# Optimization experiments

Hardware: AMD Instinct MI355X
Metric: run time of the kernel (lower is better)

The kernel has to match this reference:

```python
import jax, jax.numpy as jnp
import numpy as np

D_MODEL = 512
H = 8
DK = D_MODEL // H  # 64


def setup_inputs() -> dict:
    key = jax.random.key(0)
    ks = jax.random.split(key, 8)
    B, S = 2, 4096
    q = jax.random.normal(ks[0], (B, S, D_MODEL), dtype=jnp.float32)
    k = jax.random.normal(ks[1], (B, S, D_MODEL), dtype=jnp.float32)
    v = jax.random.normal(ks[2], (B, S, D_MODEL), dtype=jnp.float32)
    # per-head projection weights, torch nn.Linear layout [out, in], stacked over heads
    scale = 1.0 / np.sqrt(D_MODEL)
    Wq = jax.random.uniform(ks[3], (H, DK, D_MODEL), jnp.float32, -scale, scale)
    Wk = jax.random.uniform(ks[4], (H, DK, D_MODEL), jnp.float32, -scale, scale)
    Wv = jax.random.uniform(ks[5], (H, DK, D_MODEL), jnp.float32, -scale, scale)
    Wo = jax.random.uniform(ks[6], (D_MODEL, D_MODEL), jnp.float32, -scale, scale)
    # causal mask (True = keep), matches masked_fill(mask.logical_not(), -inf)
    mask = jnp.tril(jnp.ones((S, S), dtype=jnp.bool_))
    return {"q": q, "k": k, "v": v, "Wq": Wq, "Wk": Wk, "Wv": Wv, "Wo": Wo, "mask": mask}


def reference(q, k, v, Wq, Wk, Wv, Wo, mask):
    # per-head projections (stacked): x @ W^T for each head -> [B, H, S, DK]
    qh = jnp.einsum('bsd,hed->bhse', q, Wq)
    kh = jnp.einsum('bsd,hed->bhse', k, Wk)
    vh = jnp.einsum('bsd,hed->bhse', v, Wv)
    scaling = 1.0 / np.sqrt(DK)
    scores = jnp.einsum('bhse,bhte->bhst', qh, kh) * scaling  # [B,H,S,S]
    scores = jnp.where(mask, scores, -jnp.inf)
    attn = jax.nn.softmax(scores, axis=-1)
    heads = jnp.einsum('bhst,bhte->bhse', attn, vh)  # [B,H,S,DK]
    B, _, S, _ = heads.shape
    concat = jnp.transpose(heads, (0, 2, 1, 3)).reshape(B, S, D_MODEL)
    return concat @ Wo.T
```

## Files before the change

kernel.cpp:

```cpp
#include <hip/hip_runtime.h>
#include <hip/hip_bf16.h>
#include <math.h>

typedef __bf16 bf16_t;
typedef __bf16 bf16x8 __attribute__((ext_vector_type(8)));
typedef __bf16 bf16x4 __attribute__((ext_vector_type(4)));
typedef short short4v __attribute__((ext_vector_type(4)));
typedef float f32x4 __attribute__((ext_vector_type(4)));

__device__ __forceinline__ f32x4 mfma_k32(bf16x8 a, bf16x8 b, f32x4 c) {
    return __builtin_amdgcn_mfma_f32_16x16x32_bf16(a, b, c, 0, 0, 0);
}

__device__ __forceinline__ f32x4 mfma_k16(bf16x4 a, bf16x4 b, f32x4 c) {
#if __has_builtin(__builtin_amdgcn_mfma_f32_16x16x16_bf16)
    return __builtin_amdgcn_mfma_f32_16x16x16_bf16(a, b, c, 0, 0, 0);
#elif __has_builtin(__builtin_amdgcn_mfma_f32_16x16x16bf16_1k)
    short4v as, bs;
    __builtin_memcpy(&as, &a, 8);
    __builtin_memcpy(&bs, &b, 8);
    return __builtin_amdgcn_mfma_f32_16x16x16bf16_1k(as, bs, c, 0, 0, 0);
#else
    f32x4 d = c;
    asm volatile("v_mfma_f32_16x16x16_bf16 %0, %1, %2, %0" : "+v"(d) : "v"(a), "v"(b));
    return d;
#endif
}

__device__ __forceinline__ float fast_exp2(float x) {
#if __has_builtin(__builtin_amdgcn_exp2f)
    return __builtin_amdgcn_exp2f(x);
#else
    float r;
    asm("v_exp_f32 %0, %1" : "=v"(r) : "v"(x));
    return r;
#endif
}

__device__ __forceinline__ void async16(const bf16_t* g, __bf16* l) {
    __builtin_amdgcn_global_load_lds(
        (const __attribute__((address_space(1))) void*)g,
        (__attribute__((address_space(3))) void*)l, 16, 0, 0);
}

__device__ __forceinline__ int swz_col(int col, int row) {
    return (col & ~63) | ((((col >> 3) & 7) ^ (row & 7)) << 3) | (col & 7);
}

__global__ __launch_bounds__(256) void cvt_all(const float* __restrict__ q,
                                               const float* __restrict__ k,
                                               const float* __restrict__ v,
                                               const float* __restrict__ Wq,
                                               const float* __restrict__ Wk,
                                               const float* __restrict__ Wv,
                                               const float* __restrict__ Wo,
                                               bf16_t* __restrict__ qc,
                                               bf16_t* __restrict__ kc,
                                               bf16_t* __restrict__ vc,
                                               bf16_t* __restrict__ Wc) {
    const int bx = blockIdx.x;
    if (bx < 2048) {
        size_t i = ((size_t)bx * 256 + threadIdx.x) * 8;
        int row = (int)(i >> 9), col = (int)(i & 511);
        size_t di = (size_t)row * 512 + swz_col(col, row);
        float4 a0 = *(const float4*)(q + i), a1 = *(const float4*)(q + i + 4);
        float4 b0 = *(const float4*)(k + i), b1 = *(const float4*)(k + i + 4);
        float4 c0 = *(const float4*)(v + i), c1 = *(const float4*)(v + i + 4);
        bf16x8 qo, ko, vo;
        qo[0]=(__bf16)a0.x; qo[1]=(__bf16)a0.y; qo[2]=(__bf16)a0.z; qo[3]=(__bf16)a0.w;
        qo[4]=(__bf16)a1.x; qo[5]=(__bf16)a1.y; qo[6]=(__bf16)a1.z; qo[7]=(__bf16)a1.w;
        ko[0]=(__bf16)b0.x; ko[1]=(__bf16)b0.y; ko[2]=(__bf16)b0.z; ko[3]=(__bf16)b0.w;
        ko[4]=(__bf16)b1.x; ko[5]=(__bf16)b1.y; ko[6]=(__bf16)b1.z; ko[7]=(__bf16)b1.w;
        vo[0]=(__bf16)c0.x; vo[1]=(__bf16)c0.y; vo[2]=(__bf16)c0.z; vo[3]=(__bf16)c0.w;
        vo[4]=(__bf16)c1.x; vo[5]=(__bf16)c1.y; vo[6]=(__bf16)c1.z; vo[7]=(__bf16)c1.w;
        *(bf16x8*)(qc + di) = qo;
        *(bf16x8*)(kc + di) = ko;
        *(bf16x8*)(vc + di) = vo;
    } else {
        const int b2 = bx - 2048;
        const int m = b2 >> 7;
        const float* src = m == 0 ? Wq : m == 1 ? Wk : m == 2 ? Wv : Wo;
        const float sc = (m == 0) ? 0.125f * 1.44269504088896f : 1.0f;
        size_t i = ((size_t)(b2 & 127) * 256 + threadIdx.x) * 8;
        int row = (int)(i >> 9), col = (int)(i & 511);
        float4 a0 = *(const float4*)(src + i), a1 = *(const float4*)(src + i + 4);
        bf16x8 o;
        o[0]=(__bf16)(a0.x*sc); o[1]=(__bf16)(a0.y*sc); o[2]=(__bf16)(a0.z*sc); o[3]=(__bf16)(a0.w*sc);
        o[4]=(__bf16)(a1.x*sc); o[5]=(__bf16)(a1.y*sc); o[6]=(__bf16)(a1.z*sc); o[7]=(__bf16)(a1.w*sc);
        *(bf16x8*)(Wc + (size_t)m * 262144 + (size_t)row * 512 + swz_col(col, row)) = o;
    }
}

template<int MODE>
__device__ __forceinline__ void gemm128_body(const bf16_t* __restrict__ A,
                                             const bf16_t* __restrict__ B,
                                             void* __restrict__ outp,
                                             int m0, int n0) {
    __shared__ __bf16 Asm[128 * 64];
    __shared__ __bf16 Bsm[128 * 64];
    const int tid  = threadIdx.x;
    const int wave = tid >> 6;
    const int lane = tid & 63;
    const int quad = lane >> 4;
    const int l16  = lane & 15;
    const int swz  = l16 & 7;
    const int r8 = lane >> 3;
    const int c8 = (lane & 7) * 8;
    const int mrow0 = (wave & 1) * 64;
    const int ncol0 = (wave >> 1) * 64;

    f32x4 acc[4][4];
    for (int i = 0; i < 4; ++i)
        for (int j = 0; j < 4; ++j) acc[i][j] = (f32x4){0.f, 0.f, 0.f, 0.f};

    for (int kt = 0; kt < 512; kt += 64) {
        __syncthreads();
        for (int j = 0; j < 4; ++j) {
            async16(A + (size_t)(m0 + wave * 32 + j * 8 + r8) * 512 + kt + c8,
                    &Asm[(wave * 32 + j * 8) * 64]);
            async16(B + (size_t)(n0 + wave * 32 + j * 8 + r8) * 512 + kt + c8,
                    &Bsm[(wave * 32 + j * 8) * 64]);
        }
        __syncthreads();

        for (int ks = 0; ks < 2; ++ks) {
            bf16x8 af[4];
            for (int mt = 0; mt < 4; ++mt)
                af[mt] = *(const bf16x8*)&Asm[(mrow0 + mt * 16 + l16) * 64 + ((ks * 4 + quad) ^ swz) * 8];
            for (int nt = 0; nt < 4; ++nt) {
                bf16x8 bf = *(const bf16x8*)&Bsm[(ncol0 + nt * 16 + l16) * 64 + ((ks * 4 + quad) ^ swz) * 8];
                for (int mt = 0; mt < 4; ++mt)
                    acc[mt][nt] = mfma_k32(af[mt], bf, acc[mt][nt]);
            }
        }
    }

    if (MODE == 0) {
        bf16_t* out = (bf16_t*)outp;
        for (int nt = 0; nt < 4; ++nt) {
            int e = n0 + ncol0 + nt * 16 + l16;
            int h = e >> 6, el = e & 63;
            for (int mt = 0; mt < 4; ++mt)
                for (int r = 0; r < 4; ++r) {
                    int row = m0 + mrow0 + mt * 16 + quad * 4 + r;
                    int b = row >> 12, s = row & 4095;
                    int elp = (((el >> 3) ^ (row & 7)) << 3) | (el & 7);
                    out[(((size_t)(b * 8 + h)) * 4096 + s) * 64 + elp] = (bf16_t)acc[mt][nt][r];
                }
        }
    } else if (MODE == 1) {
        bf16_t* out = (bf16_t*)outp;
        for (int nt = 0; nt < 4; ++nt) {
            int s_g = n0 + ncol0 + nt * 16 + l16;
            int b = s_g >> 12;
            int sbase = (s_g & 4095) & ~63;
            int f = 16 * ((l16 >> 2) & 3) + 4 * nt + (l16 & 3);
            for (int mt = 0; mt < 4; ++mt)
                for (int r = 0; r < 4; ++r) {
                    int e_g = m0 + mrow0 + mt * 16 + quad * 4 + r;
                    int h = e_g >> 6, el = e_g & 63;
                    int col = sbase | ((((f >> 3) ^ (e_g & 7)) & 7) << 3) | (f & 7);
                    out[(((size_t)(b * 8 + h)) * 64 + el) * 4096 + col] = (bf16_t)acc[mt][nt][r];
                }
        }
    } else {
        float* out = (float*)outp;
        for (int nt = 0; nt < 4; ++nt) {
            int n = n0 + ncol0 + nt * 16 + l16;
            for (int mt = 0; mt < 4; ++mt)
                for (int r = 0; r < 4; ++r) {
                    int row = m0 + mrow0 + mt * 16 + quad * 4 + r;
                    out[(size_t)row * 512 + n] = acc[mt][nt][r];
                }
        }
    }
}

__global__ __launch_bounds__(256) void proj_fused(const bf16_t* __restrict__ xs,
                                                  const bf16_t* __restrict__ Wc,
                                                  bf16_t* __restrict__ qh,
                                                  bf16_t* __restrict__ kh,
                                                  bf16_t* __restrict__ vh) {
    const int z = blockIdx.z;
    const bf16_t* X = xs + (size_t)z * 4194304;
    const bf16_t* W = Wc + (size_t)z * 262144;
    if (z == 0)
        gemm128_body<0>(X, W, qh, blockIdx.x * 128, blockIdx.y * 128);
    else if (z == 1)
        gemm128_body<0>(X, W, kh, blockIdx.x * 128, blockIdx.y * 128);
    else
        gemm128_body<1>(W, X, vh, blockIdx.y * 128, blockIdx.x * 128);
}

__global__ __launch_bounds__(256) void gemm_final(const bf16_t* __restrict__ A,
                                                  const bf16_t* __restrict__ B,
                                                  float* __restrict__ out) {
    gemm128_body<2>(A, B, out, blockIdx.x * 128, blockIdx.y * 128);
}

__global__ __launch_bounds__(256, 4) void attn_kernel(const bf16_t* __restrict__ qh,
                                                      const bf16_t* __restrict__ kh,
                                                      const bf16_t* __restrict__ vh,
                                                      bf16_t* __restrict__ Opart,
                                                      float* __restrict__ Lpart) {
    __shared__ __bf16 SM[16384];
    __bf16* KSM = &SM[0];
    __bf16* VSM = &SM[8192];
    float* Osc = (float*)SM;
    float* Lsc = (float*)&SM[8192];

    const int id   = blockIdx.x;
    const int bh   = ((id & 7) << 1) | ((id >> 3) & 1);
    const int pair = (id >> 4) & 31;
    const int z    = (id >> 9) & 1;

    const int tid  = threadIdx.x;
    const int wave = tid >> 6;
    const int g2   = wave >> 1;
    const int wl   = wave & 1;
    const int lane = tid & 63;
    const int quad = lane >> 4;
    const int l16  = lane & 15;
    const int swz  = l16 & 7;
    const size_t base = (size_t)bh * 4096 * 64;
    const int r8 = lane >> 3;
    const int c8 = (lane & 7) * 8;

    bf16_t* Op = Opart + (size_t)z * 4194304;
    float*  Lp = Lpart + z * 65536;

    for (int leg = 0; leg < 2; ++leg) {
        const int qt = leg ? (63 - pair) : pair;
        const int q0 = qt * 64;

        bf16x8 qf[2][2];
        for (int g = 0; g < 2; ++g) {
            const bf16_t* qp = qh + base + (size_t)(q0 + wl * 32 + g * 16 + l16) * 64;
            qf[g][0] = *(const bf16x8*)(qp + ((quad ^ swz) * 8));
            qf[g][1] = *(const bf16x8*)(qp + (((4 + quad) ^ swz) * 8));
        }

        f32x4 o[2][4];
        for (int g = 0; g < 2; ++g)
            for (int i = 0; i < 4; ++i) o[g][i] = (f32x4){0.f, 0.f, 0.f, 0.f};
        float lsum[2] = {0.f, 0.f};

        const int S  = (qt + 2) >> 1;
        const int Sh = (S + 1) >> 1;
        const int it0 = z ? Sh : 0;
        const int it1 = z ? S : Sh;

        for (int it = it0; it < it1; ++it) {
            const int j0 = it * 128;
            __syncthreads();
            for (int p = 0; p < 2; ++p)
                for (int j = 0; j < 2; ++j) {
                    int row = wave * 16 + j * 8 + r8;
                    async16(kh + base + (size_t)(j0 + p * 64 + row) * 64 + c8,
                            KSM + (p * 64 + wave * 16 + j * 8) * 64);
                    async16(vh + (size_t)(bh * 64 + row) * 4096 + j0 + p * 64 + c8,
                            VSM + (p * 64 + wave * 16 + j * 8) * 64);
                }
            __syncthreads();

            const int pp = g2;
            const int koff = j0 + pp * 64 - q0;
            if (koff > wl * 32 + 31) continue;

            f32x4 st[2][4];
            for (int nt = 0; nt < 4; ++nt) {
                const __bf16* kr = KSM + (pp * 64 + nt * 16 + l16) * 64;
                bf16x8 kf0 = *(const bf16x8*)(kr + ((quad ^ swz) * 8));
                bf16x8 kf1 = *(const bf16x8*)(kr + (((4 + quad) ^ swz) * 8));
                for (int g = 0; g < 2; ++g) {
                    f32x4 zz = (f32x4){0.f, 0.f, 0.f, 0.f};
                    zz = mfma_k32(kf0, qf[g][0], zz);
                    zz = mfma_k32(kf1, qf[g][1], zz);
                    st[g][nt] = zz;
                }
            }

            bf16x4 pf[2][4];
            for (int g = 0; g < 2; ++g) {
                const int qb = wl * 32 + g * 16;
                if (koff + 63 <= qb) {
                    for (int nt = 0; nt < 4; ++nt)
                        for (int r = 0; r < 4; ++r) {
                            float p = fast_exp2(st[g][nt][r]);
                            lsum[g] += p;
                            pf[g][nt][r] = (bf16_t)p;
                        }
                } else {
                    const int qrow = qb + l16;
                    for (int nt = 0; nt < 4; ++nt)
                        for (int r = 0; r < 4; ++r) {
                            int key = nt * 16 + quad * 4 + r;
                            float p = (key + koff <= qrow) ? fast_exp2(st[g][nt][r]) : 0.f;
                            lsum[g] += p;
                            pf[g][nt][r] = (bf16_t)p;
                        }
                }
            }

            for (int dt = 0; dt < 4; ++dt)
                for (int kt2 = 0; kt2 < 2; ++kt2) {
                    bf16x8 vf = *(const bf16x8*)&VSM[(pp * 64 + dt * 16 + l16) * 64 + (((2 * quad + kt2) ^ swz) * 8)];
                    bf16x4 vlo = {vf[0], vf[1], vf[2], vf[3]};
                    bf16x4 vhi = {vf[4], vf[5], vf[6], vf[7]};
                    for (int g = 0; g < 2; ++g) {
                        o[g][dt] = mfma_k16(pf[g][2 * kt2], vlo, o[g][dt]);
                        o[g][dt] = mfma_k16(pf[g][2 * kt2 + 1], vhi, o[g][dt]);
                    }
                }
        }

        __syncthreads();
        if (g2 == 1) {
            for (int g = 0; g < 2; ++g) {
                float ls = lsum[g];
                ls += __shfl_xor(ls, 16);
                ls += __shfl_xor(ls, 32);
                const int qb = wl * 32 + g * 16;
                Lsc[qb + l16] = ls;
                for (int dt = 0; dt < 4; ++dt)
                    for (int r = 0; r < 4; ++r)
                        Osc[(qb + quad * 4 + r) * 64 + dt * 16 + l16] = o[g][dt][r];
            }
        }
        __syncthreads();
        if (g2 == 0) {
            for (int g = 0; g < 2; ++g) {
                float ls = lsum[g];
                ls += __shfl_xor(ls, 16);
                ls += __shfl_xor(ls, 32);
                const int qb = wl * 32 + g * 16;
                ls += Lsc[qb + l16];
                Lsc[qb + l16] = ls;
                for (int dt = 0; dt < 4; ++dt)
                    for (int r = 0; r < 4; ++r) {
                        int idx = (qb + quad * 4 + r) * 64 + dt * 16 + l16;
                        Osc[idx] = o[g][dt][r] + Osc[idx];
                    }
            }
        }
        __syncthreads();
        {
            const int q  = tid >> 2;
            const int e0 = (tid & 3) * 16;
            bf16x8 w0, w1;
            for (int i = 0; i < 8; ++i) {
                w0[i] = (bf16_t)Osc[q * 64 + e0 + i];
                w1[i] = (bf16_t)Osc[q * 64 + e0 + 8 + i];
            }
            size_t slot = ((size_t)(bh * 64 + qt)) * 4096 + q * 64 + e0;
            *(bf16x8*)&Op[slot]     = w0;
            *(bf16x8*)&Op[slot + 8] = w1;
            if (tid < 64) Lp[(bh * 64 + qt) * 64 + tid] = Lsc[tid];
        }
    }
}

__global__ __launch_bounds__(256) void attn_combine(const bf16_t* __restrict__ Opart,
                                                    const float* __restrict__ Lpart,
                                                    bf16_t* __restrict__ ao) {
    const int unit = blockIdx.x * 4 + (threadIdx.x >> 6);
    const int q    = threadIdx.x & 63;
    const int bh = unit >> 6, qt = unit & 63;
    const int b = bh >> 3, h = bh & 7;
    const size_t ro = (size_t)unit * 4096 + q * 64;

    float o[64];
    const bf16x8* p0 = (const bf16x8*)(Opart + ro);
    const bf16x8* p1 = (const bf16x8*)(Opart + 4194304 + ro);
    for (int c = 0; c < 8; ++c) {
        bf16x8 a = p0[c], bb = p1[c];
        for (int i = 0; i < 8; ++i) o[c * 8 + i] = (float)a[i] + (float)bb[i];
    }
    float L = Lpart[unit * 64 + q] + Lpart[65536 + unit * 64 + q];
    float inv = 1.0f / L;
    int s_g = qt * 64 + q, sw = s_g & 7;
    size_t rowoff = ((size_t)(b * 4096 + s_g)) * 512 + h * 64;
    for (int c = 0; c < 8; ++c) {
        int e0 = (c ^ sw) * 8;
        bf16x8 w;
        for (int i = 0; i < 8; ++i) w[i] = (bf16_t)(o[e0 + i] * inv);
        *(bf16x8*)&ao[rowoff + c * 8] = w;
    }
}

extern "C" void kernel_launch(void* const* d_in, const int* in_sizes, int n_in,
                              void* d_out, int out_size, void* d_ws, size_t ws_size,
                              hipStream_t stream) {
    const float* q  = (const float*)d_in[0];
    const float* k  = (const float*)d_in[1];
    const float* v  = (const float*)d_in[2];
    const float* Wq = (const float*)d_in[3];
    const float* Wk = (const float*)d_in[4];
    const float* Wv = (const float*)d_in[5];
    const float* Wo = (const float*)d_in[6];
    float* out = (float*)d_out;

    bf16_t* ws = (bf16_t*)d_ws;
    const size_t R = (size_t)8192 * 512;
    bf16_t* qc = ws;
    bf16_t* kc = ws + R;
    bf16_t* vc = ws + 2 * R;
    bf16_t* vh = ws + 3 * R;
    bf16_t* Wc = ws + 4 * R;
    float*  Lp = (float*)(ws + 4 * R + 1048576);
    bf16_t* qh = (bf16_t*)d_out;
    bf16_t* kh = (bf16_t*)d_out + R;
    bf16_t* ao = qc;

    cvt_all<<<dim3(2560), dim3(256), 0, stream>>>(q, k, v, Wq, Wk, Wv, Wo, qc, kc, vc, Wc);
    proj_fused<<<dim3(64, 4, 3), dim3(256), 0, stream>>>(ws, Wc, qh, kh, vh);
    attn_kernel<<<dim3(1024), dim3(256), 0, stream>>>(qh, kh, vh, kc, Lp);
    attn_combine<<<dim3(256), dim3(256), 0, stream>>>(kc, Lp, ao);
    gemm_final<<<dim3(64, 4), dim3(256), 0, stream>>>(ao, Wc + 3 * 262144, out);
}
```

Measured before the change: 253.1 us.

## Use K=32 MFMA for PV and compute row sums via MFMA with ones

Replaces the pair of 16x16x16 MFMAs in the P·V product with a single 16x16x32 MFMA by packing the probabilities as bf16x8. The per-row softmax denominators are now accumulated with extra MFMAs against a vector of ones, replacing the scalar adds and the cross-lane shuffles. The output scratch uses a padded row stride of 65 to reduce LDS bank conflicts, and Lsc is moved so it does not overlap the padded area. Loops are explicitly unrolled. The trade is four extra MFMAs per iteration and denominators summed from bf16-rounded probabilities.

```diff
diff --git a/kernel.cpp b/kernel.cpp
--- a/kernel.cpp
+++ b/kernel.cpp
@@ -4,27 +4,10 @@
 
 typedef __bf16 bf16_t;
 typedef __bf16 bf16x8 __attribute__((ext_vector_type(8)));
-typedef __bf16 bf16x4 __attribute__((ext_vector_type(4)));
-typedef short short4v __attribute__((ext_vector_type(4)));
 typedef float f32x4 __attribute__((ext_vector_type(4)));
 
 __device__ __forceinline__ f32x4 mfma_k32(bf16x8 a, bf16x8 b, f32x4 c) {
     return __builtin_amdgcn_mfma_f32_16x16x32_bf16(a, b, c, 0, 0, 0);
-}
-
-__device__ __forceinline__ f32x4 mfma_k16(bf16x4 a, bf16x4 b, f32x4 c) {
-#if __has_builtin(__builtin_amdgcn_mfma_f32_16x16x16_bf16)
-    return __builtin_amdgcn_mfma_f32_16x16x16_bf16(a, b, c, 0, 0, 0);
-#elif __has_builtin(__builtin_amdgcn_mfma_f32_16x16x16bf16_1k)
-    short4v as, bs;
-    __builtin_memcpy(&as, &a, 8);
-    __builtin_memcpy(&bs, &b, 8);
-    return __builtin_amdgcn_mfma_f32_16x16x16bf16_1k(as, bs, c, 0, 0, 0);
-#else
-    f32x4 d = c;
-    asm volatile("v_mfma_f32_16x16x16_bf16 %0, %1, %2, %0" : "+v"(d) : "v"(a), "v"(b));
-    return d;
-#endif
 }
 
 __device__ __forceinline__ float fast_exp2(float x) {
@@ -207,7 +190,7 @@
     __bf16* KSM = &SM[0];
     __bf16* VSM = &SM[8192];
     float* Osc = (float*)SM;
-    float* Lsc = (float*)&SM[8192];
+    float* Lsc = (float*)&SM[8320];
 
     const int id   = blockIdx.x;
     const int bh   = ((id & 7) << 1) | ((id >> 3) & 1);
@@ -226,6 +209,10 @@
     const int r8 = lane >> 3;
     const int c8 = (lane & 7) * 8;
 
+    bf16x8 ones8;
+#pragma unroll
+    for (int i = 0; i < 8; ++i) ones8[i] = (bf16_t)1.0f;
+
     bf16_t* Op = Opart + (size_t)z * 4194304;
     float*  Lp = Lpart + z * 65536;
 
@@ -243,7 +230,7 @@
         f32x4 o[2][4];
         for (int g = 0; g < 2; ++g)
             for (int i = 0; i < 4; ++i) o[g][i] = (f32x4){0.f, 0.f, 0.f, 0.f};
-        float lsum[2] = {0.f, 0.f};
+        f32x4 lacc[2] = {(f32x4){0.f, 0.f, 0.f, 0.f}, (f32x4){0.f, 0.f, 0.f, 0.f}};
 
         const int S  = (qt + 2) >> 1;
         const int Sh = (S + 1) >> 1;
@@ -268,10 +255,12 @@
             if (koff > wl * 32 + 31) continue;
 
             f32x4 st[2][4];
+#pragma unroll
             for (int nt = 0; nt < 4; ++nt) {
                 const __bf16* kr = KSM + (pp * 64 + nt * 16 + l16) * 64;
                 bf16x8 kf0 = *(const bf16x8*)(kr + ((quad ^ swz) * 8));
                 bf16x8 kf1 = *(const bf16x8*)(kr + (((4 + quad) ^ swz) * 8));
+#pragma unroll
                 for (int g = 0; g < 2; ++g) {
                     f32x4 zz = (f32x4){0.f, 0.f, 0.f, 0.f};
                     zz = mfma_k32(kf0, qf[g][0], zz);
@@ -280,65 +269,71 @@
                 }
             }
 
-            bf16x4 pf[2][4];
+            bf16x8 pf8[2][2];
+#pragma unroll
             for (int g = 0; g < 2; ++g) {
                 const int qb = wl * 32 + g * 16;
                 if (koff + 63 <= qb) {
+#pragma unroll
                     for (int nt = 0; nt < 4; ++nt)
+#pragma unroll
                         for (int r = 0; r < 4; ++r) {
                             float p = fast_exp2(st[g][nt][r]);
-                            lsum[g] += p;
-                            pf[g][nt][r] = (bf16_t)p;
+                            pf8[g][nt >> 1][(nt & 1) * 4 + r] = (bf16_t)p;
                         }
                 } else {
                     const int qrow = qb + l16;
+#pragma unroll
                     for (int nt = 0; nt < 4; ++nt)
+#pragma unroll
                         for (int r = 0; r < 4; ++r) {
                             int key = nt * 16 + quad * 4 + r;
                             float p = (key + koff <= qrow) ? fast_exp2(st[g][nt][r]) : 0.f;
-                            lsum[g] += p;
-                            pf[g][nt][r] = (bf16_t)p;
+                            pf8[g][nt >> 1][(nt & 1) * 4 + r] = (bf16_t)p;
                         }
                 }
             }
 
-            for (int dt = 0; dt < 4; ++dt)
+#pragma unroll
+            for (int g = 0; g < 2; ++g) {
+                lacc[g] = mfma_k32(pf8[g][0], ones8, lacc[g]);
+                lacc[g] = mfma_k32(pf8[g][1], ones8, lacc[g]);
+            }
+
+#pragma unroll
+            for (int dt = 0; dt < 4; ++dt) {
+                const __bf16* vr = VSM + (pp * 64 + dt * 16 + l16) * 64;
+#pragma unroll
                 for (int kt2 = 0; kt2 < 2; ++kt2) {
-                    bf16x8 vf = *(const bf16x8*)&VSM[(pp * 64 + dt * 16 + l16) * 64 + (((2 * quad + kt2) ^ swz) * 8)];
-                    bf16x4 vlo = {vf[0], vf[1], vf[2], vf[3]};
-                    bf16x4 vhi = {vf[4], vf[5], vf[6], vf[7]};
-                    for (int g = 0; g < 2; ++g) {
-                        o[g][dt] = mfma_k16(pf[g][2 * kt2], vlo, o[g][dt]);
-                        o[g][dt] = mfma_k16(pf[g][2 * kt2 + 1], vhi, o[g][dt]);
-                    }
-                }
+                    bf16x8 vf = *(const bf16x8*)(vr + (((2 * quad + kt2) ^ swz) * 8));
+                    o[0][dt] = mfma_k32(pf8[0][kt2], vf, o[0][dt]);
+                    o[1][dt] = mfma_k32(pf8[1][kt2], vf, o[1][dt]);
+                }
+            }
         }
 
         __syncthreads();
         if (g2 == 1) {
             for (int g = 0; g < 2; ++g) {
-                float ls = lsum[g];
-                ls += __shfl_xor(ls, 16);
-                ls += __shfl_xor(ls, 32);
                 const int qb = wl * 32 + g * 16;
-                Lsc[qb + l16] = ls;
+                if (l16 == 0)
+                    for (int r = 0; r < 4; ++r)
+                        Lsc[qb + quad * 4 + r] = lacc[g][r];
                 for (int dt = 0; dt < 4; ++dt)
                     for (int r = 0; r < 4; ++r)
-                        Osc[(qb + quad * 4 + r) * 64 + dt * 16 + l16] = o[g][dt][r];
+                        Osc[(qb + quad * 4 + r) * 65 + dt * 16 + l16] = o[g][dt][r];
             }
         }
         __syncthreads();
         if (g2 == 0) {
             for (int g = 0; g < 2; ++g) {
-                float ls = lsum[g];
-                ls += __shfl_xor(ls, 16);
-                ls += __shfl_xor(ls, 32);
                 const int qb = wl * 32 + g * 16;
-                ls += Lsc[qb + l16];
-                Lsc[qb + l16] = ls;
+                if (l16 == 0)
+                    for (int r = 0; r < 4; ++r)
+                        Lsc[qb + quad * 4 + r] += lacc[g][r];
                 for (int dt = 0; dt < 4; ++dt)
                     for (int r = 0; r < 4; ++r) {
-                        int idx = (qb + quad * 4 + r) * 64 + dt * 16 + l16;
+                        int idx = (qb + quad * 4 + r) * 65 + dt * 16 + l16;
                         Osc[idx] = o[g][dt][r] + Osc[idx];
                     }
             }
@@ -349,8 +344,8 @@
             const int e0 = (tid & 3) * 16;
             bf16x8 w0, w1;
             for (int i = 0; i < 8; ++i) {
-                w0[i] = (bf16_t)Osc[q * 64 + e0 + i];
-                w1[i] = (bf16_t)Osc[q * 64 + e0 + 8 + i];
+                w0[i] = (bf16_t)Osc[q * 65 + e0 + i];
+                w1[i] = (bf16_t)Osc[q * 65 + e0 + 8 + i];
             }
             size_t slot = ((size_t)(bh * 64 + qt)) * 4096 + q * 64 + e0;
             *(bf16x8*)&Op[slot]     = w0;
```

Measured after the change: 273.2 us. 1.08x slower.
